# Optimization experiments

Hardware: AMD Instinct MI355X
Metric: run time of the kernel (lower is better)

## Reference

```python
import jax, jax.numpy as jnp
import numpy as np

DIM = 1024
N_STATE = 64
T, B = 512, 32


def _xavier(key, shape):
    fan_out, fan_in = shape
    limit = np.sqrt(6.0 / (fan_in + fan_out)).astype(np.float32)
    return jax.random.uniform(key, shape, jnp.float32, -limit, limit)


def setup_inputs() -> dict:
    key = jax.random.key(0)
    ks = jax.random.split(key, 5)
    return {
        "x": jax.random.normal(ks[0], (T, B, DIM), jnp.float32),
        "S": jnp.zeros((B, N_STATE, N_STATE), jnp.float32),
        "W_k": _xavier(ks[1], (N_STATE, DIM)),
        "W_v": _xavier(ks[2], (N_STATE, DIM)),
        "W_q": _xavier(ks[3], (N_STATE, DIM)),
        "W_alpha": _xavier(ks[4], (N_STATE, DIM)),
        "d_alpha": jnp.full((N_STATE,), 0.1, jnp.float32),
        "b_alpha": jnp.full((N_STATE,), 2.0, jnp.float32),
    }


def reference(x, S, W_k, W_v, W_q, W_alpha, d_alpha, b_alpha):
    # Precompute all projections as batched GEMMs: [T,B,n_state]
    k = jnp.einsum("tbd,nd->tbn", x, W_k)
    v = jnp.einsum("tbd,nd->tbn", x, W_v)
    q = jnp.einsum("tbd,nd->tbn", x, W_q)
    ax = jnp.einsum("tbd,nd->tbn", x, W_alpha)

    def step(S, inp):
        k_t, v_t, q_t, ax_t = inp  # each [B, n_state]
        retrieved = jnp.einsum("bij,bj->bi", S, k_t)          # S @ k
        alpha = jax.nn.sigmoid(ax_t + d_alpha * retrieved + b_alpha)
        # S = alpha * S + (1 - alpha) * outer(v, k); alpha gates rows
        S_new = alpha[:, :, None] * S + (1.0 - alpha)[:, :, None] * (
            v_t[:, :, None] * k_t[:, None, :]
        )
        h = jnp.einsum("bij,bj->bi", S_new, q_t)              # S @ q
        out_t = h * jax.nn.silu(h)                             # self-gated output
        return S_new, out_t

    S_final, output = jax.lax.scan(step, S, (k, v, q, ax))
    return output, S_final
```

## Files before the change

### kernel.cpp

```cpp
#include <hip/hip_runtime.h>
#include <hip/hip_bf16.h>

#define T_STEPS 512
#define BATCH 32
#define NST 64
#define DIM 1024

typedef _Float16 f16x8 __attribute__((ext_vector_type(8)));
typedef _Float16 f16x4 __attribute__((ext_vector_type(4)));
typedef _Float16 f16x2 __attribute__((ext_vector_type(2)));
typedef float f32x4 __attribute__((ext_vector_type(4)));

__device__ __forceinline__ void gl_lds16(const void* g, void* l) {
  __builtin_amdgcn_global_load_lds(
      (const __attribute__((address_space(1))) void*)g,
      (__attribute__((address_space(3))) void*)l, 16, 0, 0);
}

__global__ __launch_bounds__(256) void wconv(
    const float* __restrict__ Wk, const float* __restrict__ Wv,
    const float* __restrict__ Wq, const float* __restrict__ Wa,
    _Float16* __restrict__ Wc) {
  const int n = blockIdx.x;
  const int g = n >> 6, r = n & 63;
  const float* W = (g == 0) ? Wk : (g == 1) ? Wq : (g == 2) ? Wv : Wa;
  float4 v = *(const float4*)(W + (size_t)r * DIM + threadIdx.x * 4);
  f16x4 h = {(_Float16)v.x, (_Float16)v.y, (_Float16)v.z, (_Float16)v.w};
  *(f16x4*)(Wc + (size_t)n * DIM + threadIdx.x * 4) = h;
}

__global__ __launch_bounds__(256) void proj_gemm(
    const float* __restrict__ x, const _Float16* __restrict__ Wc,
    _Float16* __restrict__ projh) {
  const int m0 = blockIdx.x * 64;
  const int n0 = blockIdx.y * 128;
  const int tid = threadIdx.x;
  const int lane = tid & 63, wv = tid >> 6;
  const int wm = wv >> 1, wn = wv & 1;
  const int fm = lane & 15, fq = lane >> 4;

  __shared__ __align__(16) _Float16 Al[64 * 40];
  __shared__ __align__(16) _Float16 Bl[2][128 * 32];

  const int bro = wv * 32 + (lane >> 2);
  const int bchunk = (lane & 3) ^ ((lane >> 3) & 3);
  const _Float16* gB = Wc + (size_t)(n0 + bro) * DIM + bchunk * 8;
  const int bl_off = bro * 32 + (lane & 3) * 8;

  const int arow = tid >> 2;
  const int acol = (tid & 3) * 8;
  const float* gA = x + (size_t)(m0 + arow) * DIM + acol;

  f32x4 acc[2][4];
#pragma unroll
  for (int mi = 0; mi < 2; ++mi)
#pragma unroll
    for (int ni = 0; ni < 4; ++ni) acc[mi][ni] = (f32x4){0.f, 0.f, 0.f, 0.f};

#define STAGE_B(buf, k0)                                       \
  {                                                            \
    _Pragma("unroll") for (int j = 0; j < 2; ++j)              \
        gl_lds16(gB + (size_t)j * 16 * DIM + (k0),             \
                 &Bl[buf][bl_off + j * 16 * 32]);              \
  }
  float4 xa, xb;
#define LOAD_A(k0)                          \
  {                                         \
    xa = *(const float4*)(gA + (k0));       \
    xb = *(const float4*)(gA + (k0) + 4);   \
  }

  STAGE_B(0, 0);
  LOAD_A(0);
  const int aswz = (fq ^ ((fm >> 1) & 3)) * 8;
  for (int kt = 0; kt < 32; ++kt) {
    __syncthreads();
    f16x8 ah;
    ah[0] = (_Float16)xa.x; ah[1] = (_Float16)xa.y;
    ah[2] = (_Float16)xa.z; ah[3] = (_Float16)xa.w;
    ah[4] = (_Float16)xb.x; ah[5] = (_Float16)xb.y;
    ah[6] = (_Float16)xb.z; ah[7] = (_Float16)xb.w;
    *(f16x8*)&Al[arow * 40 + acol] = ah;
    __syncthreads();
    if (kt + 1 < 32) {
      LOAD_A(kt * 32 + 32);
      STAGE_B((kt + 1) & 1, kt * 32 + 32);
    }
    f16x8 afr[2], bfr[4];
#pragma unroll
    for (int mi = 0; mi < 2; ++mi)
      afr[mi] = *(const f16x8*)&Al[(wm * 32 + mi * 16 + fm) * 40 + fq * 8];
#pragma unroll
    for (int ni = 0; ni < 4; ++ni) {
      const int row = wn * 64 + ni * 16 + fm;
      bfr[ni] = *(const f16x8*)&Bl[kt & 1][row * 32 + aswz];
    }
#pragma unroll
    for (int mi = 0; mi < 2; ++mi)
#pragma unroll
      for (int ni = 0; ni < 4; ++ni)
        acc[mi][ni] =
            __builtin_amdgcn_mfma_f32_16x16x32_f16(afr[mi], bfr[ni], acc[mi][ni], 0, 0, 0);
  }
#undef STAGE_B
#undef LOAD_A

#pragma unroll
  for (int mi = 0; mi < 2; ++mi)
#pragma unroll
    for (int ni = 0; ni < 4; ++ni) {
      const int gcol = n0 + wn * 64 + ni * 16 + fm;
      const int pcol = gcol < 128 ? gcol
                     : (gcol < 192 ? 128 + 2 * (gcol - 128) : 129 + 2 * (gcol - 192));
#pragma unroll
      for (int r = 0; r < 4; ++r) {
        const int grow = m0 + wm * 32 + mi * 16 + fq * 4 + r;
        projh[(size_t)grow * 256 + pcol] = (_Float16)acc[mi][ni][r];
      }
    }
}

__device__ __forceinline__ float red16(float x) {
  int v = __builtin_amdgcn_update_dpp(0, __float_as_int(x), 0xB1, 0xF, 0xF, true);
  x += __int_as_float(v);
  v = __builtin_amdgcn_update_dpp(0, __float_as_int(x), 0x4E, 0xF, 0xF, true);
  x += __int_as_float(v);
  v = __builtin_amdgcn_update_dpp(0, __float_as_int(x), 0x124, 0xF, 0xF, true);
  x += __int_as_float(v);
  v = __builtin_amdgcn_update_dpp(0, __float_as_int(x), 0x128, 0xF, 0xF, true);
  x += __int_as_float(v);
  return x;
}

__global__ __launch_bounds__(256) void scan_kernel(
    const _Float16* __restrict__ projh, const float* __restrict__ S0,
    const float* __restrict__ d_alpha, const float* __restrict__ b_alpha,
    float* __restrict__ out, float* __restrict__ Sout) {
  const int b = blockIdx.x >> 2;
  const int rg = blockIdx.x & 3;
  const int tid = threadIdx.x;
  const int c = tid & 15;
  const int r = rg * 16 + (tid >> 4);
  const int j0 = c * 4;

  __shared__ __align__(16) _Float16 lbuf[2 * 2048];

  float s[4];
  {
    float4 v = *(const float4*)(S0 + ((size_t)b * NST + r) * NST + j0);
    s[0] = v.x; s[1] = v.y; s[2] = v.z; s[3] = v.w;
  }
  const float da = d_alpha[r];
  const float ba = b_alpha[r];

  const _Float16* gp = projh + (size_t)b * 256;
  const int lidx = (tid >> 5) * 256 + (tid & 31) * 8;
#define GADDR(ch) (gp + (size_t)((ch) * 8 + (tid >> 5)) * (BATCH * 256) + (tid & 31) * 8)

  float4 rA;
  rA = *(const float4*)GADDR(0); *(float4*)(lbuf + lidx) = rA;
  rA = *(const float4*)GADDR(1); *(float4*)(lbuf + 2048 + lidx) = rA;
  rA = *(const float4*)GADDR(2);
  __syncthreads();

  f16x4 kf[2], qf[2];
  f16x2 vaf[2];
#define PREF(tn)                                                           \
  {                                                                        \
    const int pp = (tn)&1;                                                 \
    const _Float16* Pn = lbuf + (((tn) >> 3) & 1) * 2048 + ((tn)&7) * 256; \
    kf[pp] = *(const f16x4*)(Pn + j0);                                     \
    qf[pp] = *(const f16x4*)(Pn + 64 + j0);                                \
    vaf[pp] = *(const f16x2*)(Pn + 128 + 2 * r);                           \
  }

  PREF(0);
  for (int ch = 0; ch < 64; ++ch) {
#pragma unroll
    for (int si = 0; si < 8; ++si) {
      const int t = ch * 8 + si;
      const int p = t & 1;
      if (t + 1 < T_STEPS) PREF(t + 1);

      const float k0 = (float)kf[p][0], k1 = (float)kf[p][1];
      const float k2 = (float)kf[p][2], k3 = (float)kf[p][3];
      const float q0 = (float)qf[p][0], q1 = (float)qf[p][1];
      const float q2 = (float)qf[p][2], q3 = (float)qf[p][3];
      const float vi = (float)vaf[p][0];
      const float axv = (float)vaf[p][1];

      const float pa = fmaf(s[0], k0, s[1] * k1);
      const float pb = fmaf(s[2], k2, s[3] * k3);
      const float rr = red16(pa + pb);

      float z = fmaf(da, rr, axv + ba);
      z = fminf(fmaxf(z, -30.f), 30.f);
      const float e = __expf(-z);
      const float al = __builtin_amdgcn_rcpf(1.f + e);
      const float cc = (e * vi) * al;

      s[0] = fmaf(al, s[0], cc * k0);
      s[1] = fmaf(al, s[1], cc * k1);
      s[2] = fmaf(al, s[2], cc * k2);
      s[3] = fmaf(al, s[3], cc * k3);
      const float ha = fmaf(s[0], q0, s[1] * q1);
      const float hb = fmaf(s[2], q2, s[3] * q3);
      const float h = red16(ha + hb);

      if (c == 0) {
        const float sg = __builtin_amdgcn_rcpf(1.f + __expf(-h));
        out[((size_t)t * BATCH + b) * NST + r] = h * h * sg;
      }
    }
    if (ch + 2 < 64) {
      __syncthreads();
      *(float4*)(lbuf + (ch & 1) * 2048 + lidx) = rA;
      if (ch + 3 < 64) rA = *(const float4*)GADDR(ch + 3);
      __syncthreads();
    }
  }
#undef PREF
#undef GADDR

  float4 o = {s[0], s[1], s[2], s[3]};
  *(float4*)(Sout + ((size_t)b * NST + r) * NST + j0) = o;
}

extern "C" void kernel_launch(void* const* d_in, const int* in_sizes, int n_in,
                              void* d_out, int out_size, void* d_ws, size_t ws_size,
                              hipStream_t stream) {
  const float* x  = (const float*)d_in[0];
  const float* S0 = (const float*)d_in[1];
  const float* Wk = (const float*)d_in[2];
  const float* Wv = (const float*)d_in[3];
  const float* Wq = (const float*)d_in[4];
  const float* Wa = (const float*)d_in[5];
  const float* da = (const float*)d_in[6];
  const float* ba = (const float*)d_in[7];

  float* out  = (float*)d_out;
  float* Sout = out + (size_t)T_STEPS * BATCH * NST;
  _Float16* projh = (_Float16*)d_ws;
  _Float16* Wc = (_Float16*)((char*)d_ws + (size_t)16384 * 256 * 2);

  wconv<<<256, 256, 0, stream>>>(Wk, Wv, Wq, Wa, Wc);
  dim3 ggrid(16384 / 64, 2);
  proj_gemm<<<ggrid, 256, 0, stream>>>(x, Wc, projh);
  scan_kernel<<<4 * BATCH, 256, 0, stream>>>(projh, S0, da, ba, out, Sout);
}
```

Measured before the change: 226.0 us.

## Break scan dependency chain using precomputed consecutive-key dot products

Adds a small kernel that precomputes k_{t-1}·k_t per batch and time step. The scan uses it to obtain S_t k_{t+1} algebraically from the previous state, so the retrieval reduction for the next step can overlap the current output reduction rather than sitting on the serial critical path. The sigmoid is also rewritten with exp2 and pre-scaled constants. The cost is an extra kernel launch, a deeper register prefetch ring and a skewed, harder-to-verify recurrence whose numerics differ slightly.

```diff
diff --git a/kernel.cpp b/kernel.cpp
--- a/kernel.cpp
+++ b/kernel.cpp
@@ -120,6 +120,25 @@
     }
 }
 
+__global__ __launch_bounds__(256) void gram_kernel(
+    const _Float16* __restrict__ projh, float* __restrict__ gmat) {
+  const int b = blockIdx.x >> 1;
+  const int t = (blockIdx.x & 1) * 256 + threadIdx.x;
+  float acc = 0.f;
+  if (t > 0) {
+    const _Float16* ka = projh + ((size_t)(t - 1) * BATCH + b) * 256;
+    const _Float16* kb = projh + ((size_t)t * BATCH + b) * 256;
+#pragma unroll
+    for (int j = 0; j < 64; j += 8) {
+      f16x8 va = *(const f16x8*)(ka + j);
+      f16x8 vb = *(const f16x8*)(kb + j);
+#pragma unroll
+      for (int e = 0; e < 8; ++e) acc = fmaf((float)va[e], (float)vb[e], acc);
+    }
+  }
+  gmat[(size_t)b * T_STEPS + t] = acc;
+}
+
 __device__ __forceinline__ float red16(float x) {
   int v = __builtin_amdgcn_update_dpp(0, __float_as_int(x), 0xB1, 0xF, 0xF, true);
   x += __int_as_float(v);
@@ -133,7 +152,8 @@
 }
 
 __global__ __launch_bounds__(256) void scan_kernel(
-    const _Float16* __restrict__ projh, const float* __restrict__ S0,
+    const _Float16* __restrict__ projh, const float* __restrict__ gmat,
+    const float* __restrict__ S0,
     const float* __restrict__ d_alpha, const float* __restrict__ b_alpha,
     float* __restrict__ out, float* __restrict__ Sout) {
   const int b = blockIdx.x >> 2;
@@ -144,73 +164,106 @@
   const int j0 = c * 4;
 
   __shared__ __align__(16) _Float16 lbuf[2 * 2048];
+  __shared__ __align__(8) float glds[T_STEPS];
 
   float s[4];
   {
     float4 v = *(const float4*)(S0 + ((size_t)b * NST + r) * NST + j0);
     s[0] = v.x; s[1] = v.y; s[2] = v.z; s[3] = v.w;
   }
-  const float da = d_alpha[r];
-  const float ba = b_alpha[r];
+  constexpr float NL2E = -1.44269504088896340736f;
+  const float da2 = d_alpha[r] * NL2E;
+  const float ba2 = b_alpha[r] * NL2E;
 
   const _Float16* gp = projh + (size_t)b * 256;
   const int lidx = (tid >> 5) * 256 + (tid & 31) * 8;
 #define GADDR(ch) (gp + (size_t)((ch) * 8 + (tid >> 5)) * (BATCH * 256) + (tid & 31) * 8)
 
+  {
+    float2 g2 = *(const float2*)(gmat + (size_t)b * T_STEPS + tid * 2);
+    *(float2*)(glds + tid * 2) = g2;
+  }
   float4 rA;
   rA = *(const float4*)GADDR(0); *(float4*)(lbuf + lidx) = rA;
   rA = *(const float4*)GADDR(1); *(float4*)(lbuf + 2048 + lidx) = rA;
   rA = *(const float4*)GADDR(2);
   __syncthreads();
 
-  f16x4 kf[2], qf[2];
-  f16x2 vaf[2];
-#define PREF(tn)                                                           \
-  {                                                                        \
-    const int pp = (tn)&1;                                                 \
-    const _Float16* Pn = lbuf + (((tn) >> 3) & 1) * 2048 + ((tn)&7) * 256; \
-    kf[pp] = *(const f16x4*)(Pn + j0);                                     \
-    qf[pp] = *(const f16x4*)(Pn + 64 + j0);                                \
-    vaf[pp] = *(const f16x2*)(Pn + 128 + 2 * r);                           \
+  f16x4 kf[4], qf[4];
+  f16x2 vaf[4];
+  float gv[4];
+#define PREF(tn)                                                             \
+  {                                                                          \
+    const int pp = (tn) & 3;                                                 \
+    const _Float16* Pn = lbuf + (((tn) >> 3) & 1) * 2048 + ((tn) & 7) * 256; \
+    kf[pp] = *(const f16x4*)(Pn + j0);                                       \
+    qf[pp] = *(const f16x4*)(Pn + 64 + j0);                                  \
+    vaf[pp] = *(const f16x2*)(Pn + 128 + 2 * r);                             \
+    gv[pp] = glds[(tn)];                                                     \
   }
 
   PREF(0);
+  PREF(1);
+  qf[3] = qf[0];
+
+  float kc[4];
+  kc[0] = (float)kf[0][0]; kc[1] = (float)kf[0][1];
+  kc[2] = (float)kf[0][2]; kc[3] = (float)kf[0][3];
+  float u;
+  {
+    const float pa = fmaf(s[1], kc[1], s[0] * kc[0]);
+    const float pb = fmaf(s[3], kc[3], s[2] * kc[2]);
+    u = red16(pa + pb);
+  }
+  float al = 1.f, e = 0.f, vp = 0.f;
+  float cck[4] = {0.f, 0.f, 0.f, 0.f};
+
   for (int ch = 0; ch < 64; ++ch) {
 #pragma unroll
     for (int si = 0; si < 8; ++si) {
       const int t = ch * 8 + si;
-      const int p = t & 1;
-      if (t + 1 < T_STEPS) PREF(t + 1);
-
-      const float k0 = (float)kf[p][0], k1 = (float)kf[p][1];
-      const float k2 = (float)kf[p][2], k3 = (float)kf[p][3];
-      const float q0 = (float)qf[p][0], q1 = (float)qf[p][1];
-      const float q2 = (float)qf[p][2], q3 = (float)qf[p][3];
-      const float vi = (float)vaf[p][0];
+      const int p = si & 3;
+      const int pn1 = (si + 1) & 3;
+      const int pm1 = (si + 3) & 3;
+      if (t + 2 < T_STEPS) PREF(t + 2);
+
       const float axv = (float)vaf[p][1];
-
-      const float pa = fmaf(s[0], k0, s[1] * k1);
-      const float pb = fmaf(s[2], k2, s[3] * k3);
-      const float rr = red16(pa + pb);
-
-      float z = fmaf(da, rr, axv + ba);
-      z = fminf(fmaxf(z, -30.f), 30.f);
-      const float e = __expf(-z);
-      const float al = __builtin_amdgcn_rcpf(1.f + e);
-      const float cc = (e * vi) * al;
-
-      s[0] = fmaf(al, s[0], cc * k0);
-      s[1] = fmaf(al, s[1], cc * k1);
-      s[2] = fmaf(al, s[2], cc * k2);
-      s[3] = fmaf(al, s[3], cc * k3);
-      const float ha = fmaf(s[0], q0, s[1] * q1);
-      const float hb = fmaf(s[2], q2, s[3] * q3);
+      const float vt = (float)vaf[p][0];
+      const float w = fmaf(e, vp * gv[p], u);
+      const float rr = al * w;
+      float z2 = fmaf(da2, rr, fmaf(axv, NL2E, ba2));
+      z2 = fminf(fmaxf(z2, -43.3f), 43.3f);
+      const float eN = __builtin_amdgcn_exp2f(z2);
+      const float alN = __builtin_amdgcn_rcpf(1.f + eN);
+      const float ccN = (eN * vt) * alN;
+
+      s[0] = fmaf(al, s[0], cck[0]);
+      s[1] = fmaf(al, s[1], cck[1]);
+      s[2] = fmaf(al, s[2], cck[2]);
+      s[3] = fmaf(al, s[3], cck[3]);
+
+      float kn[4];
+      kn[0] = (float)kf[pn1][0]; kn[1] = (float)kf[pn1][1];
+      kn[2] = (float)kf[pn1][2]; kn[3] = (float)kf[pn1][3];
+      const float ua = fmaf(s[1], kn[1], s[0] * kn[0]);
+      const float ub = fmaf(s[3], kn[3], s[2] * kn[2]);
+      const float uN = red16(ua + ub);
+
+      const float q0 = (float)qf[pm1][0], q1 = (float)qf[pm1][1];
+      const float q2 = (float)qf[pm1][2], q3 = (float)qf[pm1][3];
+      const float ha = fmaf(s[1], q1, s[0] * q0);
+      const float hb = fmaf(s[3], q3, s[2] * q2);
       const float h = red16(ha + hb);
-
-      if (c == 0) {
-        const float sg = __builtin_amdgcn_rcpf(1.f + __expf(-h));
-        out[((size_t)t * BATCH + b) * NST + r] = h * h * sg;
+      if (c == 0 && t > 0) {
+        const float sg =
+            __builtin_amdgcn_rcpf(1.f + __builtin_amdgcn_exp2f(h * NL2E));
+        out[((size_t)(t - 1) * BATCH + b) * NST + r] = (h * h) * sg;
       }
+
+      cck[0] = ccN * kc[0]; cck[1] = ccN * kc[1];
+      cck[2] = ccN * kc[2]; cck[3] = ccN * kc[3];
+      kc[0] = kn[0]; kc[1] = kn[1]; kc[2] = kn[2]; kc[3] = kn[3];
+      al = alN; e = eN; vp = vt; u = uN;
     }
     if (ch + 2 < 64) {
       __syncthreads();
@@ -222,6 +275,22 @@
 #undef PREF
 #undef GADDR
 
+  s[0] = fmaf(al, s[0], cck[0]);
+  s[1] = fmaf(al, s[1], cck[1]);
+  s[2] = fmaf(al, s[2], cck[2]);
+  s[3] = fmaf(al, s[3], cck[3]);
+  {
+    const float q0 = (float)qf[3][0], q1 = (float)qf[3][1];
+    const float q2 = (float)qf[3][2], q3 = (float)qf[3][3];
+    const float ha = fmaf(s[1], q1, s[0] * q0);
+    const float hb = fmaf(s[3], q3, s[2] * q2);
+    const float h = red16(ha + hb);
+    if (c == 0) {
+      const float sg =
+          __builtin_amdgcn_rcpf(1.f + __builtin_amdgcn_exp2f(h * NL2E));
+      out[((size_t)(T_STEPS - 1) * BATCH + b) * NST + r] = (h * h) * sg;
+    }
+  }
   float4 o = {s[0], s[1], s[2], s[3]};
   *(float4*)(Sout + ((size_t)b * NST + r) * NST + j0) = o;
 }
@@ -242,9 +311,11 @@
   float* Sout = out + (size_t)T_STEPS * BATCH * NST;
   _Float16* projh = (_Float16*)d_ws;
   _Float16* Wc = (_Float16*)((char*)d_ws + (size_t)16384 * 256 * 2);
+  float* gmat = (float*)((char*)d_ws + (size_t)16384 * 256 * 2 + 512 * 1024);
 
   wconv<<<256, 256, 0, stream>>>(Wk, Wv, Wq, Wa, Wc);
   dim3 ggrid(16384 / 64, 2);
   proj_gemm<<<ggrid, 256, 0, stream>>>(x, Wc, projh);
-  scan_kernel<<<4 * BATCH, 256, 0, stream>>>(projh, S0, da, ba, out, Sout);
-}
+  gram_kernel<<<64, 256, 0, stream>>>(projh, gmat);
+  scan_kernel<<<4 * BATCH, 256, 0, stream>>>(projh, gmat, S0, da, ba, out, Sout);
+}
```

After: 232.9 us. 1.03x slower.

## Compute full 256-column projection per block with double-buffered A tiles

Applied to the files above, without the earlier changes.

The projection GEMM now uses 512-thread blocks that each cover all 256 output columns for a 64-row tile, instead of two blocks per row tile. Each x tile is therefore read from global memory once rather than twice. The A tile is also double-buffered in swizzled LDS, and the K loop is unrolled by two so the next A and B stages are issued before the current MFMA work, leaving one barrier per k-step. The cost is a larger LDS footprint and bigger blocks, which may reduce occupancy, and the grid shrinks to 256 blocks.

```diff
diff --git a/kernel.cpp b/kernel.cpp
--- a/kernel.cpp
+++ b/kernel.cpp
@@ -29,27 +29,46 @@
   *(f16x4*)(Wc + (size_t)n * DIM + threadIdx.x * 4) = h;
 }
 
-__global__ __launch_bounds__(256) void proj_gemm(
+__global__ __launch_bounds__(512) void proj_gemm(
     const float* __restrict__ x, const _Float16* __restrict__ Wc,
     _Float16* __restrict__ projh) {
   const int m0 = blockIdx.x * 64;
-  const int n0 = blockIdx.y * 128;
   const int tid = threadIdx.x;
   const int lane = tid & 63, wv = tid >> 6;
-  const int wm = wv >> 1, wn = wv & 1;
+  const int wm = wv >> 2, wn = wv & 3;
   const int fm = lane & 15, fq = lane >> 4;
 
-  __shared__ __align__(16) _Float16 Al[64 * 40];
-  __shared__ __align__(16) _Float16 Bl[2][128 * 32];
-
-  const int bro = wv * 32 + (lane >> 2);
-  const int bchunk = (lane & 3) ^ ((lane >> 3) & 3);
-  const _Float16* gB = Wc + (size_t)(n0 + bro) * DIM + bchunk * 8;
-  const int bl_off = bro * 32 + (lane & 3) * 8;
-
-  const int arow = tid >> 2;
-  const int acol = (tid & 3) * 8;
-  const float* gA = x + (size_t)(m0 + arow) * DIM + acol;
+  __shared__ __align__(16) _Float16 Bl[2][256 * 32];
+  __shared__ __align__(16) _Float16 Al[2][64 * 32];
+
+  const int brow = tid >> 2;
+  const int bcg = (tid & 3) ^ ((tid >> 3) & 3);
+  const _Float16* gB = Wc + (size_t)brow * DIM + bcg * 8;
+  const int bdst = tid * 8;
+
+#define STAGE_B(buf, k0)                                          \
+  {                                                               \
+    _Pragma("unroll") for (int i = 0; i < 2; ++i)                 \
+        gl_lds16(gB + (size_t)i * 128 * DIM + (k0),               \
+                 &Bl[buf][i * 4096 + bdst]);                      \
+  }
+
+  const int arow = tid >> 3;
+  const int afc = (tid & 7) * 4;
+  const float* gA = x + (size_t)(m0 + arow) * DIM + afc;
+  const int awp = arow * 32 + ((((tid >> 1) & 3) ^ ((arow >> 1) & 3)) * 8) +
+                  (tid & 1) * 4;
+
+#define LOADX(rr, k0)                          \
+  {                                            \
+    rr = *(const float4*)(gA + (k0));          \
+  }
+#define CVT_WRITE_A(buf, rr)                                        \
+  {                                                                 \
+    f16x4 h = {(_Float16)rr.x, (_Float16)rr.y, (_Float16)rr.z,      \
+               (_Float16)rr.w};                                     \
+    *(f16x4*)&Al[buf][awp] = h;                                     \
+  }
 
   f32x4 acc[2][4];
 #pragma unroll
@@ -57,59 +76,54 @@
 #pragma unroll
     for (int ni = 0; ni < 4; ++ni) acc[mi][ni] = (f32x4){0.f, 0.f, 0.f, 0.f};
 
-#define STAGE_B(buf, k0)                                       \
-  {                                                            \
-    _Pragma("unroll") for (int j = 0; j < 2; ++j)              \
-        gl_lds16(gB + (size_t)j * 16 * DIM + (k0),             \
-                 &Bl[buf][bl_off + j * 16 * 32]);              \
-  }
-  float4 xa, xb;
-#define LOAD_A(k0)                          \
-  {                                         \
-    xa = *(const float4*)(gA + (k0));       \
-    xb = *(const float4*)(gA + (k0) + 4);   \
-  }
-
+  const int aswz = (fq ^ ((fm >> 1) & 3)) * 8;
+  const int abase = (wm * 32 + fm) * 32 + aswz;
+  const int bbase = (wn * 64 + fm) * 32 + aswz;
+
+#define COMPUTE(cb)                                                     \
+  {                                                                     \
+    f16x8 afr[2], bfr[4];                                               \
+    _Pragma("unroll") for (int mi = 0; mi < 2; ++mi)                    \
+        afr[mi] = *(const f16x8*)&Al[cb][abase + mi * 16 * 32];         \
+    _Pragma("unroll") for (int ni = 0; ni < 4; ++ni)                    \
+        bfr[ni] = *(const f16x8*)&Bl[cb][bbase + ni * 16 * 32];         \
+    _Pragma("unroll") for (int mi = 0; mi < 2; ++mi)                    \
+        _Pragma("unroll") for (int ni = 0; ni < 4; ++ni)                \
+            acc[mi][ni] = __builtin_amdgcn_mfma_f32_16x16x32_f16(       \
+                afr[mi], bfr[ni], acc[mi][ni], 0, 0, 0);                \
+  }
+
+  float4 rE, rO;
+  LOADX(rE, 0);
   STAGE_B(0, 0);
-  LOAD_A(0);
-  const int aswz = (fq ^ ((fm >> 1) & 3)) * 8;
-  for (int kt = 0; kt < 32; ++kt) {
+  LOADX(rO, 32);
+  CVT_WRITE_A(0, rE);
+  __syncthreads();
+
+  for (int k2 = 0; k2 < 16; ++k2) {
+    STAGE_B(1, (2 * k2 + 1) * 32);
+    if (k2 < 15) LOADX(rE, (2 * k2 + 2) * 32);
+    CVT_WRITE_A(1, rO);
+    COMPUTE(0);
     __syncthreads();
-    f16x8 ah;
-    ah[0] = (_Float16)xa.x; ah[1] = (_Float16)xa.y;
-    ah[2] = (_Float16)xa.z; ah[3] = (_Float16)xa.w;
-    ah[4] = (_Float16)xb.x; ah[5] = (_Float16)xb.y;
-    ah[6] = (_Float16)xb.z; ah[7] = (_Float16)xb.w;
-    *(f16x8*)&Al[arow * 40 + acol] = ah;
+    if (k2 < 15) {
+      STAGE_B(0, (2 * k2 + 2) * 32);
+      LOADX(rO, (2 * k2 + 3) * 32);
+      CVT_WRITE_A(0, rE);
+    }
+    COMPUTE(1);
     __syncthreads();
-    if (kt + 1 < 32) {
-      LOAD_A(kt * 32 + 32);
-      STAGE_B((kt + 1) & 1, kt * 32 + 32);
-    }
-    f16x8 afr[2], bfr[4];
-#pragma unroll
-    for (int mi = 0; mi < 2; ++mi)
-      afr[mi] = *(const f16x8*)&Al[(wm * 32 + mi * 16 + fm) * 40 + fq * 8];
+  }
+#undef STAGE_B
+#undef LOADX
+#undef CVT_WRITE_A
+#undef COMPUTE
+
+#pragma unroll
+  for (int mi = 0; mi < 2; ++mi)
 #pragma unroll
     for (int ni = 0; ni < 4; ++ni) {
-      const int row = wn * 64 + ni * 16 + fm;
-      bfr[ni] = *(const f16x8*)&Bl[kt & 1][row * 32 + aswz];
-    }
-#pragma unroll
-    for (int mi = 0; mi < 2; ++mi)
-#pragma unroll
-      for (int ni = 0; ni < 4; ++ni)
-        acc[mi][ni] =
-            __builtin_amdgcn_mfma_f32_16x16x32_f16(afr[mi], bfr[ni], acc[mi][ni], 0, 0, 0);
-  }
-#undef STAGE_B
-#undef LOAD_A
-
-#pragma unroll
-  for (int mi = 0; mi < 2; ++mi)
-#pragma unroll
-    for (int ni = 0; ni < 4; ++ni) {
-      const int gcol = n0 + wn * 64 + ni * 16 + fm;
+      const int gcol = wn * 64 + ni * 16 + fm;
       const int pcol = gcol < 128 ? gcol
                      : (gcol < 192 ? 128 + 2 * (gcol - 128) : 129 + 2 * (gcol - 192));
 #pragma unroll
@@ -244,7 +258,6 @@
   _Float16* Wc = (_Float16*)((char*)d_ws + (size_t)16384 * 256 * 2);
 
   wconv<<<256, 256, 0, stream>>>(Wk, Wv, Wq, Wa, Wc);
-  dim3 ggrid(16384 / 64, 2);
-  proj_gemm<<<ggrid, 256, 0, stream>>>(x, Wc, projh);
+  proj_gemm<<<256, 512, 0, stream>>>(x, Wc, projh);
   scan_kernel<<<4 * BATCH, 256, 0, stream>>>(projh, S0, da, ba, out, Sout);
 }
```

Result: no change. 224.9 us (-0.5%).
